# Optimization experiments

Hardware: AMD Instinct MI355X
Metric: run time of the kernel (lower is better)

The kernel has to match this reference:

```python
import jax, jax.numpy as jnp
import numpy as np

EPS = 1e-6

def setup_inputs() -> dict:
    key = jax.random.key(0)
    k = jax.random.split(key, 5)
    G, in_g, out_g = 16, 64, 64
    x = jax.random.normal(k[0], (G * in_g, 8, 64, 64), dtype=jnp.float32)
    ln_gamma = 1.0 + 0.1 * jax.random.normal(k[1], (G, in_g), dtype=jnp.float32)
    ln_beta = 0.1 * jax.random.normal(k[2], (G, in_g), dtype=jnp.float32)
    W = jax.random.normal(k[3], (G, out_g, in_g), dtype=jnp.float32) / np.sqrt(in_g)
    b = 0.1 * jax.random.normal(k[4], (G, out_g), dtype=jnp.float32)
    return {"x": x, "ln_gamma": ln_gamma, "ln_beta": ln_beta, "W": W, "b": b}


def reference(x, ln_gamma, ln_beta, W, b):
    # x: [C_in, D1, D2, D3]; W: [G, out_g, in_g]; faithful to torch reshape semantics
    G, out_g, in_g = W.shape
    D1, D2, D3 = x.shape[1:]
    xg = x.reshape(G, D1, D2, D3, in_g)            # row-major reshape, same as torch
    # per-group LayerNorm over last dim (biased variance, eps=1e-6)
    mu = jnp.mean(xg, axis=-1, keepdims=True)
    var = jnp.mean(jnp.square(xg - mu), axis=-1, keepdims=True)
    xn = (xg - mu) * jax.lax.rsqrt(var + EPS)
    xn = xn * ln_gamma[:, None, None, None, :] + ln_beta[:, None, None, None, :]
    # per-group Linear: y_g = xn_g @ W_g^T + b_g  -> [G, D1, D2, D3, out_g]
    y = jnp.einsum('gabck,gok->gabco', xn, W) + b[:, None, None, None, :]
    # torch.cat(list_of_groups, dim=-1): groups become the fastest-varying blocks of last dim
    y = jnp.moveaxis(y, 0, -2).reshape(D1, D2, D3, G * out_g)
    # permute([3, 0, 1, 2]) -> [C_out, D1, D2, D3]
    return jnp.transpose(y, (3, 0, 1, 2))
```

## Files before the change

### kernel.cpp

```cpp
#include <hip/hip_runtime.h>

typedef __attribute__((ext_vector_type(4))) float f32x4;
typedef __attribute__((ext_vector_type(8))) short bf16x8;

__device__ __forceinline__ short bf16_rne(float f) {
    unsigned int u = __float_as_uint(f);
    u += 0x7FFFu + ((u >> 16) & 1u);
    return (short)(u >> 16);
}


__global__ __launch_bounds__(256, 2)
void gln_mfma_kernel(const float* __restrict__ x,
                     const float* __restrict__ gamma,
                     const float* __restrict__ beta,
                     const float* __restrict__ W,
                     const float* __restrict__ bias,
                     float* __restrict__ out)
{
    const int tid  = threadIdx.x;
    const int lane = tid & 63;
    const int w    = blockIdx.x * 4 + (tid >> 6);
    const int g    = w >> 9;
    const int rr0  = (w & 511) << 6;

    const int l15 = lane & 15;
    const int l4  = lane >> 4;
    const int ks  = l4 * 8;

    bf16x8 bfrag[4][2];
    {
        const float* Wg = W + (size_t)(g * 64) * 64;
        #pragma unroll
        for (int ot = 0; ot < 4; ++ot) {
            const float* wrow = Wg + (size_t)(ot * 16 + l15) * 64;
            #pragma unroll
            for (int kc = 0; kc < 2; ++kc) {
                f32x4 w0 = *(const f32x4*)(wrow + kc * 32 + ks);
                f32x4 w1 = *(const f32x4*)(wrow + kc * 32 + ks + 4);
                bf16x8 f;
                #pragma unroll
                for (int j = 0; j < 4; ++j) { f[j] = bf16_rne(w0[j]); f[j + 4] = bf16_rne(w1[j]); }
                bfrag[ot][kc] = f;
            }
        }
    }

    float gk[16], bk[16];
    {
        const float* gp = gamma + g * 64;
        const float* bp = beta  + g * 64;
        #pragma unroll
        for (int kc = 0; kc < 2; ++kc) {
            f32x4 g0 = *(const f32x4*)(gp + kc * 32 + ks);
            f32x4 g1 = *(const f32x4*)(gp + kc * 32 + ks + 4);
            f32x4 b0 = *(const f32x4*)(bp + kc * 32 + ks);
            f32x4 b1 = *(const f32x4*)(bp + kc * 32 + ks + 4);
            #pragma unroll
            for (int j = 0; j < 4; ++j) {
                gk[kc * 8 + j] = g0[j]; gk[kc * 8 + 4 + j] = g1[j];
                bk[kc * 8 + j] = b0[j]; bk[kc * 8 + 4 + j] = b1[j];
            }
        }
    }

    float bo[4];
    #pragma unroll
    for (int ot = 0; ot < 4; ++ot) bo[ot] = bias[g * 64 + ot * 16 + l15];

    const float* xg = x   + (size_t)g * 32768 * 64;
    float* outg     = out + (size_t)g * 64 * 32768;

    f32x4 buf[2][4];
    {
        const float* rowp = xg + (size_t)(rr0 + l15) * 64;
        buf[0][0] = *(const f32x4*)(rowp + ks);
        buf[0][1] = *(const f32x4*)(rowp + ks + 4);
        buf[0][2] = *(const f32x4*)(rowp + 32 + ks);
        buf[0][3] = *(const f32x4*)(rowp + 32 + ks + 4);
    }

    f32x4 vout[4][4];

    #pragma unroll
    for (int t = 0; t < 4; ++t) {
        if (t + 1 < 4) {
            const float* rowp = xg + (size_t)(rr0 + (t + 1) * 16 + l15) * 64;
            buf[(t + 1) & 1][0] = *(const f32x4*)(rowp + ks);
            buf[(t + 1) & 1][1] = *(const f32x4*)(rowp + ks + 4);
            buf[(t + 1) & 1][2] = *(const f32x4*)(rowp + 32 + ks);
            buf[(t + 1) & 1][3] = *(const f32x4*)(rowp + 32 + ks + 4);
        }

        float s = 0.f, s2 = 0.f;
        #pragma unroll
        for (int i = 0; i < 4; ++i) {
            #pragma unroll
            for (int j = 0; j < 4; ++j) {
                float v = buf[t & 1][i][j];
                s += v; s2 += v * v;
            }
        }
        s  += __shfl_xor(s, 16, 64);  s  += __shfl_xor(s, 32, 64);
        s2 += __shfl_xor(s2, 16, 64); s2 += __shfl_xor(s2, 32, 64);
        const float mu   = s * (1.0f / 64.0f);
        const float var  = s2 * (1.0f / 64.0f) - mu * mu;
        const float rstd = rsqrtf(var + 1e-6f);

        bf16x8 a0, a1;
        #pragma unroll
        for (int j = 0; j < 8; ++j) {
            float c1 = rstd * gk[j];
            float v  = buf[t & 1][j >> 2][j & 3] * c1 + (bk[j] - mu * c1);
            a0[j] = bf16_rne(v);
        }
        #pragma unroll
        for (int j = 0; j < 8; ++j) {
            float c1 = rstd * gk[8 + j];
            float v  = buf[t & 1][2 + (j >> 2)][j & 3] * c1 + (bk[8 + j] - mu * c1);
            a1[j] = bf16_rne(v);
        }

        #pragma unroll
        for (int ot = 0; ot < 4; ++ot) {
            f32x4 acc = {0.f, 0.f, 0.f, 0.f};
            acc = __builtin_amdgcn_mfma_f32_16x16x32_bf16(a0, bfrag[ot][0], acc, 0, 0, 0);
            acc = __builtin_amdgcn_mfma_f32_16x16x32_bf16(a1, bfrag[ot][1], acc, 0, 0, 0);
            #pragma unroll
            for (int q = 0; q < 4; ++q) acc[q] += bo[ot];
            vout[t][ot] = acc;
        }
    }

    #pragma unroll
    for (int ot = 0; ot < 4; ++ot) {
        float* base = outg + (size_t)(ot * 16 + l15) * 32768 + rr0 + l4 * 4;
        #pragma unroll
        for (int t = 0; t < 4; ++t) {
            __builtin_nontemporal_store(vout[t][ot], (f32x4*)(base + t * 16));
        }
    }
}

extern "C" void kernel_launch(void* const* d_in, const int* in_sizes, int n_in,
                              void* d_out, int out_size, void* d_ws, size_t ws_size,
                              hipStream_t stream) {
    const float* x     = (const float*)d_in[0];
    const float* gamma = (const float*)d_in[1];
    const float* beta  = (const float*)d_in[2];
    const float* W     = (const float*)d_in[3];
    const float* b     = (const float*)d_in[4];
    float* out = (float*)d_out;

    dim3 grid(2048), block(256);
    hipLaunchKernelGGL(gln_mfma_kernel, grid, block, 0, stream, x, gamma, beta, W, b, out);
}
```

Before: 61.19 us.

## Split output channels across two waves per row tile to double parallelism

Each 64-row tile is now handled by two waves, each computing half of the 64 output channels, and the grid is doubled. This lowers per-wave register use (fewer weight fragments and accumulators) and raises occupancy and memory-level parallelism. The cost is that each x row tile is loaded and normalised twice, adding redundant input traffic (likely absorbed by L2) and duplicated LayerNorm work.

New measurement: 76.40 us. 1.25x slower.

```diff
diff --git a/kernel.cpp b/kernel.cpp
--- a/kernel.cpp
+++ b/kernel.cpp
@@ -21,19 +21,24 @@
     const int tid  = threadIdx.x;
     const int lane = tid & 63;
     const int w    = blockIdx.x * 4 + (tid >> 6);
-    const int g    = w >> 9;
-    const int rr0  = (w & 511) << 6;
+    const int p    = w >> 1;
+    const int h    = w & 1;
+    const int g    = p >> 9;
+    const int rr0  = (p & 511) << 6;
 
     const int l15 = lane & 15;
     const int l4  = lane >> 4;
     const int ks  = l4 * 8;
 
-    bf16x8 bfrag[4][2];
+    const float* xg = x   + (size_t)g * 32768 * 64;
+    float* outg     = out + (size_t)g * 64 * 32768;
+
+    bf16x8 bfrag[2][2];
     {
         const float* Wg = W + (size_t)(g * 64) * 64;
         #pragma unroll
-        for (int ot = 0; ot < 4; ++ot) {
-            const float* wrow = Wg + (size_t)(ot * 16 + l15) * 64;
+        for (int oti = 0; oti < 2; ++oti) {
+            const float* wrow = Wg + (size_t)((h * 2 + oti) * 16 + l15) * 64;
             #pragma unroll
             for (int kc = 0; kc < 2; ++kc) {
                 f32x4 w0 = *(const f32x4*)(wrow + kc * 32 + ks);
@@ -41,7 +46,7 @@
                 bf16x8 f;
                 #pragma unroll
                 for (int j = 0; j < 4; ++j) { f[j] = bf16_rne(w0[j]); f[j + 4] = bf16_rne(w1[j]); }
-                bfrag[ot][kc] = f;
+                bfrag[oti][kc] = f;
             }
         }
     }
@@ -64,12 +69,9 @@
         }
     }
 
-    float bo[4];
+    float bo[2];
     #pragma unroll
-    for (int ot = 0; ot < 4; ++ot) bo[ot] = bias[g * 64 + ot * 16 + l15];
-
-    const float* xg = x   + (size_t)g * 32768 * 64;
-    float* outg     = out + (size_t)g * 64 * 32768;
+    for (int oti = 0; oti < 2; ++oti) bo[oti] = bias[g * 64 + (h * 2 + oti) * 16 + l15];
 
     f32x4 buf[2][4];
     {
@@ -80,7 +82,7 @@
         buf[0][3] = *(const f32x4*)(rowp + 32 + ks + 4);
     }
 
-    f32x4 vout[4][4];
+    f32x4 vout[4][2];
 
     #pragma unroll
     for (int t = 0; t < 4; ++t) {
@@ -122,22 +124,22 @@
         }
 
         #pragma unroll
-        for (int ot = 0; ot < 4; ++ot) {
+        for (int oti = 0; oti < 2; ++oti) {
             f32x4 acc = {0.f, 0.f, 0.f, 0.f};
-            acc = __builtin_amdgcn_mfma_f32_16x16x32_bf16(a0, bfrag[ot][0], acc, 0, 0, 0);
-            acc = __builtin_amdgcn_mfma_f32_16x16x32_bf16(a1, bfrag[ot][1], acc, 0, 0, 0);
+            acc = __builtin_amdgcn_mfma_f32_16x16x32_bf16(a0, bfrag[oti][0], acc, 0, 0, 0);
+            acc = __builtin_amdgcn_mfma_f32_16x16x32_bf16(a1, bfrag[oti][1], acc, 0, 0, 0);
             #pragma unroll
-            for (int q = 0; q < 4; ++q) acc[q] += bo[ot];
-            vout[t][ot] = acc;
+            for (int q = 0; q < 4; ++q) acc[q] += bo[oti];
+            vout[t][oti] = acc;
         }
     }
 
     #pragma unroll
-    for (int ot = 0; ot < 4; ++ot) {
-        float* base = outg + (size_t)(ot * 16 + l15) * 32768 + rr0 + l4 * 4;
+    for (int oti = 0; oti < 2; ++oti) {
+        float* base = outg + (size_t)((h * 2 + oti) * 16 + l15) * 32768 + rr0 + l4 * 4;
         #pragma unroll
         for (int t = 0; t < 4; ++t) {
-            __builtin_nontemporal_store(vout[t][ot], (f32x4*)(base + t * 16));
+            __builtin_nontemporal_store(vout[t][oti], (f32x4*)(base + t * 16));
         }
     }
 }
@@ -152,6 +154,6 @@
     const float* b     = (const float*)d_in[4];
     float* out = (float*)d_out;
 
-    dim3 grid(2048), block(256);
+    dim3 grid(4096), block(256);
     hipLaunchKernelGGL(gln_mfma_kernel, grid, block, 0, stream, x, gamma, beta, W, b, out);
 }
```
